# Kernel optimization log

Hardware: AMD Instinct MI355X
Metric: run time of the kernel (lower is better)

## Reference

```python
import jax, jax.numpy as jnp
import numpy as np

HIDDEN = 2048
HEADS = 16
HEAD_DIM = HIDDEN // HEADS
LATENT = 512
B, T = 2, 2048


def setup_inputs() -> dict:
    key = jax.random.key(0)
    ks = jax.random.split(key, 12)
    s = lambda fan_in: 1.0 / np.sqrt(fan_in)
    x = jax.random.normal(ks[0], (B, T, HIDDEN), dtype=jnp.float32)
    Wq = jax.random.uniform(ks[1], (HIDDEN, HIDDEN), jnp.float32, -s(HIDDEN), s(HIDDEN))
    bq = jax.random.uniform(ks[2], (HIDDEN,), jnp.float32, -s(HIDDEN), s(HIDDEN))
    Wl = jax.random.uniform(ks[3], (HIDDEN, LATENT), jnp.float32, -s(HIDDEN), s(HIDDEN))
    bl = jax.random.uniform(ks[4], (LATENT,), jnp.float32, -s(HIDDEN), s(HIDDEN))
    # per-head back-projections stacked along head axis: [H, latent, head_dim]
    Wk = jax.random.uniform(ks[5], (HEADS, LATENT, HEAD_DIM), jnp.float32, -s(LATENT), s(LATENT))
    bk = jax.random.uniform(ks[6], (HEADS, HEAD_DIM), jnp.float32, -s(LATENT), s(LATENT))
    Wv = jax.random.uniform(ks[7], (HEADS, LATENT, HEAD_DIM), jnp.float32, -s(LATENT), s(LATENT))
    bv = jax.random.uniform(ks[8], (HEADS, HEAD_DIM), jnp.float32, -s(LATENT), s(LATENT))
    Wo = jax.random.uniform(ks[9], (HIDDEN, HIDDEN), jnp.float32, -s(HIDDEN), s(HIDDEN))
    bo = jax.random.uniform(ks[10], (HIDDEN,), jnp.float32, -s(HIDDEN), s(HIDDEN))
    return {"x": x, "Wq": Wq, "bq": bq, "Wl": Wl, "bl": bl,
            "Wk": Wk, "bk": bk, "Wv": Wv, "bv": bv, "Wo": Wo, "bo": bo}


def reference(x, Wq, bq, Wl, bl, Wk, bk, Wv, bv, Wo, bo):
    Bc, Tc, _ = x.shape
    # Q projection, split into heads: [B, H, T, Dh]
    q = (x @ Wq + bq).reshape(Bc, Tc, HEADS, HEAD_DIM).transpose(0, 2, 1, 3)
    # shared low-rank latent KV (cache=None -> just new tokens): [B, T, L]
    latent = x @ Wl + bl
    # per-head back-projections fused as one grouped matmul: [B, H, T, Dh]
    k = jnp.einsum('btl,hld->bhtd', latent, Wk) + bk[None, :, None, :]
    v = jnp.einsum('btl,hld->bhtd', latent, Wv) + bv[None, :, None, :]
    # full (non-causal) attention, matching the original module
    scores = jnp.einsum('bhqd,bhkd->bhqk', q, k) / np.sqrt(HEAD_DIM).astype(jnp.float32)
    probs = jax.nn.softmax(scores, axis=-1)
    attn = jnp.einsum('bhqk,bhkd->bhqd', probs, v)
    attn = attn.transpose(0, 2, 1, 3).reshape(Bc, Tc, HIDDEN)
    return attn @ Wo + bo
```

## Files before the change

### kernel.cpp

```cpp
#include <hip/hip_runtime.h>
#include <hip/hip_bf16.h>
#include <cstdint>

#define SEQ     2048
#define NHID    2048
#define NLAT    512
#define NHEAD   16
#define DHEAD   128
#define NBATCH  2
#define NROWS   (NBATCH*SEQ)

typedef unsigned short u16;
typedef __attribute__((ext_vector_type(8))) short short8;
typedef __attribute__((ext_vector_type(4))) float f32x4;

#define MFMA16 __builtin_amdgcn_mfma_f32_16x16x32_bf16

#define QSCALE 0.12751743f

#if __has_builtin(__builtin_amdgcn_exp2f)
#define EXP2(x) __builtin_amdgcn_exp2f(x)
#else
#define EXP2(x) __expf((x) * 0.6931471805599453f)
#endif

__device__ __forceinline__ u16 f2b(float f) {
    uint32_t u = __float_as_uint(f);
    uint32_t r = (u + 0x7fffu + ((u >> 16) & 1u)) >> 16;
    return (u16)r;
}

__device__ __forceinline__ uint32_t cvt_pk_bf16(float a, float b) {
    uint32_t r;
    asm("v_cvt_pk_bf16_f32 %0, %1, %2" : "=v"(r) : "v"(a), "v"(b));
    return r;
}

__device__ __forceinline__ void async16(const u16* g, u16* l) {
    __builtin_amdgcn_global_load_lds(
        (const __attribute__((address_space(1))) unsigned int*)g,
        (__attribute__((address_space(3))) unsigned int*)l, 16, 0, 0);
}

__device__ __forceinline__ void stage_lds(const u16* __restrict__ src, size_t strideE,
                                          u16* lds, int wave, int lane,
                                          int log2cpr, int xmask, int xshift,
                                          int reps, int nlanes) {
    const int cmask = (1 << log2cpr) - 1;
    for (int rep = 0; rep < reps; ++rep) {
        int cbase = rep * nlanes + wave * 64;
        int ci = cbase + lane;
        int row = ci >> log2cpr;
        int sc = ci & cmask;
        int dchunk = sc ^ ((row >> xshift) & xmask);
        const u16* g = src + (size_t)row * strideE + dchunk * 8;
        async16(g, lds + (size_t)cbase * 8);
    }
}

__global__ __launch_bounds__(256) void prep(const float* __restrict__ x,
                                            const float* __restrict__ Wq,
                                            const float* __restrict__ Wl,
                                            const float* __restrict__ Wk,
                                            const float* __restrict__ Wv,
                                            const float* __restrict__ Wo,
                                            u16* __restrict__ xb,
                                            u16* __restrict__ WqlT,
                                            u16* __restrict__ WkvT,
                                            u16* __restrict__ WoT) {
    const int t = blockIdx.x, tid = threadIdx.x;
    if (t < 8192) {
        int i = t * 256 + tid;
        float4 v = ((const float4*)x)[i];
        unsigned int lo = (unsigned int)f2b(v.x) | ((unsigned int)f2b(v.y) << 16);
        unsigned int hi = (unsigned int)f2b(v.z) | ((unsigned int)f2b(v.w) << 16);
        ((uint2*)xb)[i] = make_uint2(lo, hi);
        return;
    }
    __shared__ float tile[32][33];
    const float* src; u16* dst; int R, C, tY, tX;
    if (t < 12288)      { int tt = t - 8192;  src = Wq; dst = WqlT;           R = 2048; C = 2048; tY = tt >> 6; tX = tt & 63; }
    else if (t < 13312) { int tt = t - 12288; src = Wl; dst = WqlT + 4194304; R = 2048; C = 512;  tY = tt >> 4; tX = tt & 15; }
    else if (t < 14336) { int tt = t - 13312; int hh = tt >> 6; tt &= 63;
                          src = Wk + hh * 65536; dst = WkvT + hh * 65536;     R = 512;  C = 128;  tY = tt >> 2; tX = tt & 3; }
    else if (t < 15360) { int tt = t - 14336; int hh = tt >> 6; tt &= 63;
                          src = Wv + hh * 65536; dst = WkvT + 1048576 + hh * 65536;
                                                                              R = 512;  C = 128;  tY = tt >> 2; tX = tt & 3; }
    else                { int tt = t - 15360; src = Wo; dst = WoT;            R = 2048; C = 2048; tY = tt >> 6; tX = tt & 63; }
    const int tx = tid & 31, ty = tid >> 5;
    const int r0 = tY * 32, c0 = tX * 32;
    #pragma unroll
    for (int i = 0; i < 32; i += 8)
        tile[ty + i][tx] = src[(size_t)(r0 + ty + i) * C + c0 + tx];
    __syncthreads();
    #pragma unroll
    for (int i = 0; i < 32; i += 8)
        dst[(size_t)(c0 + ty + i) * R + r0 + tx] = f2b(tile[tx][ty + i]);
}

template<int STORE>
__global__ __launch_bounds__(256) void gemm_bt(const u16* __restrict__ A,
                                               const u16* __restrict__ Bt,
                                               const float* __restrict__ bias1,
                                               const float* __restrict__ bias2,
                                               void* __restrict__ C1,
                                               void* __restrict__ C2,
                                               int M, int N, int K) {
    __shared__ __align__(16) u16 As[2][128 * 32];
    __shared__ __align__(16) u16 Bs[2][128 * 32];
    const int tid = threadIdx.x, wave = tid >> 6, lane = tid & 63;
    const int quad = lane >> 4, m16 = lane & 15;
    const int m0 = blockIdx.y * 128, n0 = blockIdx.x * 128;
    const int wr = wave >> 1, wc = wave & 1;
    const int swz = (quad ^ ((m16 >> 1) & 3)) * 8;
    const u16* Ab = A + (size_t)m0 * K;
    const u16* Bb = Bt + (size_t)n0 * K;
    const int KI = K >> 5;

    stage_lds(Ab, K, As[0], wave, lane, 2, 3, 1, 2, 256);
    stage_lds(Bb, K, Bs[0], wave, lane, 2, 3, 1, 2, 256);

    f32x4 acc[4][4] = {};
    for (int it = 0; it < KI; ++it) {
        const int cur = it & 1;
        __syncthreads();
        if (it + 1 < KI) {
            stage_lds(Ab + (it + 1) * 32, K, As[cur ^ 1], wave, lane, 2, 3, 1, 2, 256);
            stage_lds(Bb + (it + 1) * 32, K, Bs[cur ^ 1], wave, lane, 2, 3, 1, 2, 256);
        }
        short8 af[4], bfr[4];
        #pragma unroll
        for (int i = 0; i < 4; i++)
            af[i] = *(const short8*)&As[cur][(wr * 64 + i * 16 + m16) * 32 + swz];
        #pragma unroll
        for (int j = 0; j < 4; j++)
            bfr[j] = *(const short8*)&Bs[cur][(wc * 64 + j * 16 + m16) * 32 + swz];
        #pragma unroll
        for (int i = 0; i < 4; i++)
            #pragma unroll
            for (int j = 0; j < 4; j++)
                acc[i][j] = MFMA16(af[i], bfr[j], acc[i][j], 0, 0, 0);
    }
    const bool second = (n0 >= 2048);
    #pragma unroll
    for (int j = 0; j < 4; j++) {
        int n = n0 + wc * 64 + j * 16 + m16;
        float bv;
        if constexpr (STORE == 2) bv = bias1[n];
        else bv = second ? bias2[n - 2048] : bias1[n];
        #pragma unroll
        for (int i = 0; i < 4; i++) {
            int mrow = m0 + wr * 64 + i * 16 + quad * 4;
            if constexpr (STORE == 4) {
                if (second) {
                    int n2 = n - 2048;
                    ushort4 pkv;
                    pkv.x = f2b(acc[i][j][0] + bv);
                    pkv.y = f2b(acc[i][j][1] + bv);
                    pkv.z = f2b(acc[i][j][2] + bv);
                    pkv.w = f2b(acc[i][j][3] + bv);
                    int c = mrow & 2047;
                    c = (c & ~12) | ((c & 4) << 1) | ((c & 8) >> 1);
                    *(ushort4*)&((u16*)C2)[((size_t)((m0 >> 11) * 2048 + n2)) * 2048 + c] = pkv;
                    continue;
                }
            }
            #pragma unroll
            for (int r = 0; r < 4; r++) {
                float v = acc[i][j][r] + bv;
                int m = mrow + r;
                if constexpr (STORE == 2)
                    ((float*)C1)[(size_t)m * N + n] = v;
                else if constexpr (STORE == 3) {
                    if (!second) ((u16*)C1)[(size_t)m * 2048 + n] = f2b(v * QSCALE);
                    else         ((u16*)C2)[(size_t)m * 512 + (n - 2048)] = f2b(v);
                } else {
                    ((u16*)C1)[(size_t)m * 2048 + n] = f2b(v);
                }
            }
        }
    }
}

__global__ __launch_bounds__(256, 2) void attn_fused(const u16* __restrict__ Q,
                                                     const u16* __restrict__ Kf,
                                                     const u16* __restrict__ Vt,
                                                     u16* __restrict__ Ob) {
    __shared__ __align__(16) u16 Kt[2][64 * 128];
    __shared__ __align__(16) u16 Vtile[2][128 * 64];
    const int tid = threadIdx.x, wave = tid >> 6, lane = tid & 63;
    const int quad = lane >> 4, m16 = lane & 15;
    const int bh = blockIdx.x, b = bh >> 4, h = bh & 15;
    const int q0 = blockIdx.y * 128;
    const size_t grow = (size_t)b * SEQ;
    const u16* Kbase = Kf + grow * NHID + h * DHEAD;
    const u16* Vbase = Vt + (grow + h * DHEAD) * SEQ;

    const u16* qsrc = Q + (grow + q0) * NHID + h * DHEAD;
    stage_lds(qsrc, NHID, Kt[0], wave, lane, 4, 15, 0, 4, 256);
    stage_lds(qsrc + (size_t)64 * NHID, NHID, Kt[1], wave, lane, 4, 15, 0, 4, 256);
    __syncthreads();
    short8 qf[2][4];
    {
        const u16* qbuf = Kt[wave >> 1];
        int rbase = (wave & 1) * 32;
        #pragma unroll
        for (int i = 0; i < 2; i++)
            #pragma unroll
            for (int c = 0; c < 4; c++)
                qf[i][c] = *(const short8*)&qbuf[(rbase + i * 16 + m16) * 128 +
                                                (((c * 4 + quad) ^ m16)) * 8];
    }
    __syncthreads();

    stage_lds(Kbase, NHID, Kt[0], wave, lane, 4, 15, 0, 4, 256);
    stage_lds(Vbase, SEQ, Vtile[0], wave, lane, 3, 7, 0, 4, 256);

    f32x4 o[2][8] = {};
    float lsum[2] = {};

    for (int it = 0; it < SEQ / 64; ++it) {
        const int cur = it & 1;
        __syncthreads();
        if (it + 1 < SEQ / 64) {
            stage_lds(Kbase + (size_t)(it + 1) * 64 * NHID, NHID, Kt[cur ^ 1],
                      wave, lane, 4, 15, 0, 4, 256);
            stage_lds(Vbase + (it + 1) * 64, SEQ, Vtile[cur ^ 1],
                      wave, lane, 3, 7, 0, 4, 256);
        }
        const u16* kt = Kt[cur];
        const u16* vt = Vtile[cur];

        f32x4 s[2][4] = {};
        __builtin_amdgcn_s_setprio(1);
        #pragma unroll
        for (int c = 0; c < 4; c++)
            #pragma unroll
            for (int j = 0; j < 4; j++) {
                short8 kb = *(const short8*)&kt[(j * 16 + m16) * 128 +
                                               (((c * 4 + quad) ^ m16)) * 8];
                s[0][j] = MFMA16(kb, qf[0][c], s[0][j], 0, 0, 0);
                s[1][j] = MFMA16(kb, qf[1][c], s[1][j], 0, 0, 0);
            }
        __builtin_amdgcn_s_setprio(0);

        uint32_t pk[2][4][2];
        #pragma unroll
        for (int i = 0; i < 2; i++) {
            float rs = 0.f;
            #pragma unroll
            for (int j = 0; j < 4; j++) {
                float p0 = EXP2(s[i][j][0]);
                float p1 = EXP2(s[i][j][1]);
                float p2 = EXP2(s[i][j][2]);
                float p3 = EXP2(s[i][j][3]);
                rs += (p0 + p1) + (p2 + p3);
                pk[i][j][0] = cvt_pk_bf16(p0, p1);
                pk[i][j][1] = cvt_pk_bf16(p2, p3);
            }
            lsum[i] += rs;
        }

        __builtin_amdgcn_s_setprio(1);
        #pragma unroll
        for (int c2 = 0; c2 < 2; c2++) {
            short8 pa[2];
            #pragma unroll
            for (int i = 0; i < 2; i++) {
                union { uint32_t u[4]; short8 s8; } pu;
#if __has_builtin(__builtin_amdgcn_permlane32_swap)
                auto r0 = __builtin_amdgcn_permlane32_swap(pk[i][2 * c2][0],
                                                           pk[i][2 * c2 + 1][0],
                                                           false, false);
                auto r1 = __builtin_amdgcn_permlane32_swap(pk[i][2 * c2][1],
                                                           pk[i][2 * c2 + 1][1],
                                                           false, false);
                pu.u[0] = r0[0]; pu.u[1] = r1[0]; pu.u[2] = r0[1]; pu.u[3] = r1[1];
#else
                uint32_t jl0 = pk[i][2 * c2][0],     jl1 = pk[i][2 * c2][1];
                uint32_t jh0 = pk[i][2 * c2 + 1][0], jh1 = pk[i][2 * c2 + 1][1];
                uint32_t sl0 = __shfl_xor(jl0, 32), sl1 = __shfl_xor(jl1, 32);
                uint32_t sh0 = __shfl_xor(jh0, 32), sh1 = __shfl_xor(jh1, 32);
                const bool low = lane < 32;
                pu.u[0] = low ? jl0 : sh0;
                pu.u[1] = low ? jl1 : sh1;
                pu.u[2] = low ? sl0 : jh0;
                pu.u[3] = low ? sl1 : jh1;
#endif
                pa[i] = pu.s8;
            }
            #pragma unroll
            for (int jd = 0; jd < 8; jd++) {
                short8 vb = *(const short8*)&vt[(jd * 16 + m16) * 64 +
                                               (((c2 * 4 + quad) ^ (m16 & 7))) * 8];
                o[0][jd] = MFMA16(pa[0], vb, o[0][jd], 0, 0, 0);
                o[1][jd] = MFMA16(pa[1], vb, o[1][jd], 0, 0, 0);
            }
        }
        __builtin_amdgcn_s_setprio(0);
    }

    #pragma unroll
    for (int i = 0; i < 2; i++) {
        float v = lsum[i];
        v += __shfl_xor(v, 16);
        v += __shfl_xor(v, 32);
        lsum[i] = v;
    }
    #pragma unroll
    for (int i = 0; i < 2; i++) {
        float inv[4];
        #pragma unroll
        for (int r = 0; r < 4; r++)
            inv[r] = 1.f / __shfl(lsum[i], quad * 4 + r);
        #pragma unroll
        for (int jd = 0; jd < 8; jd++)
            #pragma unroll
            for (int r = 0; r < 4; r++) {
                int t = q0 + wave * 32 + i * 16 + quad * 4 + r;
                int d = jd * 16 + m16;
                Ob[(grow + t) * NHID + h * DHEAD + d] = f2b(o[i][jd][r] * inv[r]);
            }
    }
}

extern "C" void kernel_launch(void* const* d_in, const int* in_sizes, int n_in,
                              void* d_out, int out_size, void* d_ws, size_t ws_size,
                              hipStream_t stream) {
    const float* x  = (const float*)d_in[0];
    const float* Wq = (const float*)d_in[1];
    const float* bq = (const float*)d_in[2];
    const float* Wl = (const float*)d_in[3];
    const float* bl = (const float*)d_in[4];
    const float* Wk = (const float*)d_in[5];
    const float* bk = (const float*)d_in[6];
    const float* Wv = (const float*)d_in[7];
    const float* bv = (const float*)d_in[8];
    const float* Wo = (const float*)d_in[9];
    const float* bo = (const float*)d_in[10];
    float* out = (float*)d_out;

    u16* w = (u16*)d_ws;
    u16* xb    = w;
    u16* WqlT  = xb    + 8388608;
    u16* WkvT  = WqlT  + 5242880;
    u16* WoT   = WkvT  + 2097152;
    u16* qb    = WoT   + 4194304;
    u16* kb    = qb    + 8388608;
    u16* vt    = kb    + 8388608;
    u16* lat   = vt    + 8388608;
    u16* attnb = xb;

    prep<<<19456, 256, 0, stream>>>(x, Wq, Wl, Wk, Wv, Wo, xb, WqlT, WkvT, WoT);

    gemm_bt<3><<<dim3(20, 32), 256, 0, stream>>>(xb, WqlT, bq, bl, qb, lat,
                                                 NROWS, 2560, 2048);
    gemm_bt<4><<<dim3(32, 32), 256, 0, stream>>>(lat, WkvT, bk, bv, kb, vt,
                                                 NROWS, 4096, 512);

    attn_fused<<<dim3(32, 16), 256, 0, stream>>>(qb, kb, vt, attnb);

    gemm_bt<2><<<dim3(16, 32), 256, 0, stream>>>(attnb, WoT, bo, nullptr, out, nullptr,
                                                 NROWS, 2048, 2048);
}
```

Before: 345.0 us.

## Vectorize weight transpose-convert and remap GEMM workgroups for XCD locality

The transpose/convert kernel now loads each 32x32 fp32 tile with one float4 per thread and writes bf16 output as ushort4, instead of eight scalar loads and stores per thread. This reduces the number of memory instructions in the weight preparation pass. The GEMM kernel also remaps its linear block index so that consecutive tiles land on the same XCD, aiming to improve L2 reuse across neighbouring tiles on MI355X's chiplet layout. The new LDS access pattern for the column reads may bring some bank conflicts.

```diff
diff --git a/kernel.cpp b/kernel.cpp
--- a/kernel.cpp
+++ b/kernel.cpp
@@ -87,15 +87,25 @@
                           src = Wv + hh * 65536; dst = WkvT + 1048576 + hh * 65536;
                                                                               R = 512;  C = 128;  tY = tt >> 2; tX = tt & 3; }
     else                { int tt = t - 15360; src = Wo; dst = WoT;            R = 2048; C = 2048; tY = tt >> 6; tX = tt & 63; }
-    const int tx = tid & 31, ty = tid >> 5;
     const int r0 = tY * 32, c0 = tX * 32;
-    #pragma unroll
-    for (int i = 0; i < 32; i += 8)
-        tile[ty + i][tx] = src[(size_t)(r0 + ty + i) * C + c0 + tx];
+    {
+        const int rr = tid >> 3, c4 = tid & 7;
+        float4 v4 = *(const float4*)&src[(size_t)(r0 + rr) * C + c0 + c4 * 4];
+        tile[rr][c4 * 4 + 0] = v4.x;
+        tile[rr][c4 * 4 + 1] = v4.y;
+        tile[rr][c4 * 4 + 2] = v4.z;
+        tile[rr][c4 * 4 + 3] = v4.w;
+    }
     __syncthreads();
-    #pragma unroll
-    for (int i = 0; i < 32; i += 8)
-        dst[(size_t)(c0 + ty + i) * R + r0 + tx] = f2b(tile[tx][ty + i]);
+    {
+        const int rg = tid & 7, cc = tid >> 3;
+        ushort4 o4;
+        o4.x = f2b(tile[rg * 4 + 0][cc]);
+        o4.y = f2b(tile[rg * 4 + 1][cc]);
+        o4.z = f2b(tile[rg * 4 + 2][cc]);
+        o4.w = f2b(tile[rg * 4 + 3][cc]);
+        *(ushort4*)&dst[(size_t)(c0 + cc) * R + r0 + rg * 4] = o4;
+    }
 }
 
 template<int STORE>
@@ -110,7 +120,14 @@
     __shared__ __align__(16) u16 Bs[2][128 * 32];
     const int tid = threadIdx.x, wave = tid >> 6, lane = tid & 63;
     const int quad = lane >> 4, m16 = lane & 15;
-    const int m0 = blockIdx.y * 128, n0 = blockIdx.x * 128;
+    const int gx = gridDim.x;
+    const int nwg = gx * gridDim.y;
+    int lin = blockIdx.x + gx * blockIdx.y;
+    int xcd = lin & 7, pos = lin >> 3;
+    int qq = nwg >> 3, rr2 = nwg & 7;
+    int wg = (xcd < rr2) ? xcd * (qq + 1) + pos
+                         : rr2 * (qq + 1) + (xcd - rr2) * qq + pos;
+    const int m0 = (wg / gx) * 128, n0 = (wg % gx) * 128;
     const int wr = wave >> 1, wc = wave & 1;
     const int swz = (quad ^ ((m16 >> 1) & 3)) * 8;
     const u16* Ab = A + (size_t)m0 * K;
```

Measured after the change: 334.1 us. -3.2%, faster.
